# Kernel tuning notes

Hardware: AMD Instinct MI355X
Metric: run time of the kernel (lower is better)

## Reference

```python
import jax, jax.numpy as jnp
import numpy as np

C = 256
CQ = C // 4


def setup_inputs() -> dict:
    key = jax.random.key(0)
    ks = jax.random.split(key, 7)
    B, H, W = 4, 64, 64
    x = jax.random.normal(ks[0], (B, C, H, W), dtype=jnp.float32)
    s = 1.0 / np.sqrt(C)
    Wq = jax.random.normal(ks[1], (CQ, C), dtype=jnp.float32) * s
    bq = jnp.zeros((CQ,), dtype=jnp.float32)
    Wk = jax.random.normal(ks[2], (CQ, C), dtype=jnp.float32) * s
    bk = jnp.zeros((CQ,), dtype=jnp.float32)
    Wv = jax.random.normal(ks[3], (C, C), dtype=jnp.float32) * s
    bv = jnp.zeros((C,), dtype=jnp.float32)
    gamma = jnp.zeros((1,), dtype=jnp.float32)
    return {"x": x, "Wq": Wq, "bq": bq, "Wk": Wk, "bk": bk,
            "Wv": Wv, "bv": bv, "gamma": gamma}


def reference(x, Wq, bq, Wk, bk, Wv, bv, gamma):
    B, Cc, Hh, Ww = x.shape
    N = Hh * Ww
    xf = x.reshape(B, Cc, N)                      # [B, C, N]
    # 1x1 convs are channel-mixing matmuls
    q = jnp.einsum('oc,bcn->bon', Wq, xf) + bq[None, :, None]   # [B, C/4, N]
    k = jnp.einsum('oc,bcn->bon', Wk, xf) + bk[None, :, None]   # [B, C/4, N]
    v = jnp.einsum('oc,bcn->bon', Wv, xf) + bv[None, :, None]   # [B, C, N]
    energy = jnp.einsum('bci,bcj->bij', q, k)     # [B, N, N] (unscaled)
    attn = jax.nn.softmax(energy, axis=-1)
    out = jnp.einsum('bcj,bij->bci', v, attn)     # [B, C, N]
    out = out.reshape(B, Cc, Hh, Ww)
    return gamma[0] * out + x
```

## Files before the change

### kernel.cpp

```cpp
#include <hip/hip_runtime.h>
#include <hip/hip_bf16.h>

typedef unsigned short u16;
typedef unsigned int u32;
typedef float f32x4 __attribute__((ext_vector_type(4)));
typedef short s16x8 __attribute__((ext_vector_type(8)));

#define MFMA16(a, b, c) __builtin_amdgcn_mfma_f32_16x16x32_bf16(a, b, c, 0, 0, 0)

#define NN 4096
#define CC 256
#define CQ 64

__device__ __forceinline__ u16 f2bf(float x) {
    union { float f; u32 u; } v; v.f = x;
    return (u16)((v.u + 0x7FFFu + ((v.u >> 16) & 1u)) >> 16);
}
__device__ __forceinline__ float bf2f(u16 u) {
    union { u32 u; float f; } v; v.u = ((u32)u) << 16;
    return v.f;
}
__device__ __forceinline__ void gll16(const void* g, void* l) {
    __builtin_amdgcn_global_load_lds(
        (const __attribute__((address_space(1))) void*)g,
        (__attribute__((address_space(3))) void*)l, 16, 0, 0);
}

__global__ __launch_bounds__(256) void prep(
    const float* __restrict__ x, const float* __restrict__ Wq,
    const float* __restrict__ Wk, const float* __restrict__ Wv,
    u16* __restrict__ xT, u16* __restrict__ wbf)
{
    const int bid = blockIdx.x, t = threadIdx.x;
    if (bid < 1024) {
        __shared__ float tile[64 * 65];
        const int b = bid >> 8, ctile = (bid >> 6) & 3, ntile = bid & 63;
        const int c0 = ctile * 64, n0 = ntile * 64;
        const int cw = t >> 4, nj = (t & 15) * 4;
        for (int it = 0; it < 4; it++) {
            const int ci = it * 16 + cw;
            const float4 v4 = *(const float4*)(x + ((size_t)(b * CC + c0 + ci)) * NN + n0 + nj);
            tile[(nj + 0) * 65 + ci] = v4.x;
            tile[(nj + 1) * 65 + ci] = v4.y;
            tile[(nj + 2) * 65 + ci] = v4.z;
            tile[(nj + 3) * 65 + ci] = v4.w;
        }
        __syncthreads();
        const int r = t >> 2, c16 = (t & 3) * 16;
        union { u16 h[16]; uint4 q[2]; } pk;
        for (int j = 0; j < 16; j++) pk.h[j] = f2bf(tile[r * 65 + c16 + j]);
        u16* dst = xT + ((size_t)(b * NN + n0 + r)) * CC + c0 + c16;
        *(uint4*)dst = pk.q[0];
        *(uint4*)(dst + 8) = pk.q[1];
    } else {
        const int flat = (bid - 1024) * 1024 + t * 4;
        const int o = flat >> 8, c = flat & 255;
        const float* src = (o < 64)  ? (Wq + (size_t)o * CC + c)
                         : (o < 128) ? (Wk + (size_t)(o - 64) * CC + c)
                                     : (Wv + (size_t)(o - 128) * CC + c);
        const float4 v4 = *(const float4*)src;
        union { u16 h[4]; uint2 d; } pk;
        pk.h[0] = f2bf(v4.x); pk.h[1] = f2bf(v4.y);
        pk.h[2] = f2bf(v4.z); pk.h[3] = f2bf(v4.w);
        *(uint2*)(wbf + (size_t)o * CC + c) = pk.d;
    }
}

__global__ __launch_bounds__(512, 4) void qkv(
    const u16* __restrict__ xT, const u16* __restrict__ wbf,
    const float* __restrict__ bq, const float* __restrict__ bk,
    const float* __restrict__ bv,
    u16* __restrict__ qT, u16* __restrict__ kT, u16* __restrict__ v)
{
    __shared__ __align__(16) u16 sm[384 * 64 + 32 * 64];
    u16* Ws = sm;
    u16* Xs = sm + 384 * 64;

    const int bid = blockIdx.x;
    const int b = bid >> 7, n0 = (bid & 127) * 32;
    const int t = threadIdx.x, lane = t & 63, w = t >> 6;
    const int col = lane & 15, quad = lane >> 4;

    f32x4 acc[3][2];
    for (int i = 0; i < 3; i++) { acc[i][0] = f32x4{0,0,0,0}; acc[i][1] = f32x4{0,0,0,0}; }

    for (int cc = 0; cc < 4; cc++) {
        const int c0 = cc * 64;
        for (int m = 0; m < 6; m++) {
            const int g = m * 512 + t;
            const int row = g >> 3, ch = g & 7;
            gll16(wbf + (size_t)row * CC + c0 + ((ch ^ (row & 7)) * 8), Ws + g * 8);
        }
        if (w < 4) {
            const int g = w * 64 + lane;
            const int n = g >> 3, ch = g & 7;
            gll16(xT + ((size_t)(b * NN + n0 + n)) * CC + c0 + ((ch ^ (n & 7)) * 8),
                  Xs + g * 8);
        }
        __syncthreads();
        for (int kk = 0; kk < 2; kk++) {
            s16x8 bx[2];
            for (int nt2 = 0; nt2 < 2; nt2++) {
                const int n = nt2 * 16 + col;
                bx[nt2] = *(const s16x8*)&Xs[n * 64 + (((kk * 4 + quad) ^ (n & 7)) * 8)];
            }
            for (int ot = 0; ot < 3; ot++) {
                const int row = w * 48 + ot * 16 + col;
                const s16x8 a = *(const s16x8*)&Ws[row * 64 + (((kk * 4 + quad) ^ (row & 7)) * 8)];
                acc[ot][0] = MFMA16(a, bx[0], acc[ot][0]);
                acc[ot][1] = MFMA16(a, bx[1], acc[ot][1]);
            }
        }
        __syncthreads();
    }
    for (int ot = 0; ot < 3; ot++) {
        const int og = w * 48 + ot * 16 + quad * 4;
        for (int nt2 = 0; nt2 < 2; nt2++) {
            const int n = n0 + nt2 * 16 + col;
            if (og < 64) {
                union { u16 h[4]; uint2 d; } pk;
                for (int r = 0; r < 4; r++) pk.h[r] = f2bf(acc[ot][nt2][r] + bq[og + r]);
                *(uint2*)(qT + ((size_t)(b * NN + n)) * CQ + og) = pk.d;
            } else if (og < 128) {
                union { u16 h[4]; uint2 d; } pk;
                for (int r = 0; r < 4; r++) pk.h[r] = f2bf(acc[ot][nt2][r] + bk[og - 64 + r]);
                *(uint2*)(kT + ((size_t)(b * NN + n)) * CQ + (og - 64)) = pk.d;
            } else {
                for (int r = 0; r < 4; r++)
                    v[((size_t)(b * CC + og - 128 + r)) * NN + n] =
                        f2bf(acc[ot][nt2][r] + bv[og - 128 + r]);
            }
        }
    }
}

__global__ __launch_bounds__(512, 4) void flash_attn(
    const u16* __restrict__ qT, const u16* __restrict__ kT,
    const u16* __restrict__ v,
    u16* __restrict__ Op0, float* __restrict__ Op1,
    float* __restrict__ lws)
{
    __shared__ __align__(16) u16 sm[24576];
    __shared__ float ls[2][64];

    const int bid = blockIdx.x;
    const int p = bid & 7;
    const int b = p >> 1, jh = p & 1;
    const int n0 = (bid >> 3) * 64;
    const int jb = jh * 2048;
    const int t = threadIdx.x;
    const int lane = t & 63, wv = t >> 6;
    const int col = lane & 15, quad = lane >> 4;
    const int strip = wv & 3, jhi = wv >> 2;
    const int ih = wv >> 2, cq = wv & 3;

    const int swz8 = (quad ^ ((col >> 1) & 3)) * 8;

    s16x8 aq[2];
    {
        const u16* qp = qT + ((size_t)(b * NN + n0 + strip * 16 + col)) * CQ + quad * 8;
        aq[0] = *(const s16x8*)qp;
        aq[1] = *(const s16x8*)(qp + 32);
    }

    f32x4 o_[2][4];
    for (int i = 0; i < 2; i++) for (int j = 0; j < 4; j++) o_[i][j] = f32x4{0,0,0,0};
    float lac[4] = {0.f, 0.f, 0.f, 0.f};

    const int kg = wv * 64 + lane;
    const int krow = kg >> 3;
    const u16* ksrc = kT + ((size_t)(b * NN + jb + krow)) * CQ + (((kg & 7) ^ (krow & 7)) * 8);
    const int kdo = kg * 8;
    const u16* vsrc[2];
    int vdo[2];
    for (int m = 0; m < 2; m++) {
        const int g = m * 512 + t;
        const int row = g >> 2;
        vdo[m] = g * 8;
        vsrc[m] = v + ((size_t)(b * CC + row)) * NN + jb
                    + (((g & 3) ^ ((row >> 1) & 3)) * 8);
    }

    auto issueK = [&](int jt, int kb) {
        if (wv < 4) gll16(ksrc + (size_t)jt * 32 * CQ, sm + kb * 2048 + kdo);
    };
    auto issueV = [&](int jt, int vb) {
        u16* base = sm + 4096 + vb * 8192;
        for (int m = 0; m < 2; m++)
            gll16(vsrc[m] + jt * 32, base + vdo[m]);
    };
    auto S_phase = [&](int kb, int pb) {
        const u16* Kb = sm + kb * 2048;
        u16* Pb = sm + 20480 + pb * 2048;
        f32x4 s = f32x4{0,0,0,0};
        for (int kk = 0; kk < 2; kk++) {
            const int jrow = jhi * 16 + col;
            const s16x8 bk_ = *(const s16x8*)
                &Kb[jrow * 64 + (((kk * 4 + quad) ^ (jrow & 7)) * 8)];
            s = MFMA16(aq[kk], bk_, s);
        }
        const int jch = jhi * 2 + (col >> 3);
        const int jin = col & 7;
        for (int r = 0; r < 4; r++) {
            const float pv = __expf(fminf(s[r], 60.f));
            lac[r] += pv;
            const int rrow = strip * 16 + quad * 4 + r;
            Pb[rrow * 32 + ((jch ^ ((quad * 2 + (r >> 1)) & 3)) * 8) + jin] = f2bf(pv);
        }
    };
    auto PV_phase = [&](int pb, int vb) {
        const u16* Pb = sm + 20480 + pb * 2048;
        const u16* Vb = sm + 4096 + vb * 8192;
        s16x8 pa[2];
        for (int it2 = 0; it2 < 2; it2++)
            pa[it2] = *(const s16x8*)&Pb[((ih * 2 + it2) * 16 + col) * 32 + swz8];
        for (int ct = 0; ct < 4; ct++) {
            const int c = cq * 64 + ct * 16 + col;
            const s16x8 bv_ = *(const s16x8*)&Vb[c * 32 + swz8];
            o_[0][ct] = MFMA16(pa[0], bv_, o_[0][ct]);
            o_[1][ct] = MFMA16(pa[1], bv_, o_[1][ct]);
        }
    };

    issueK(0, 0);
    issueV(0, 0);
    issueK(1, 1);
    __syncthreads();
    S_phase(0, 0);

    int vcur = 0, pcur = 0;
    for (int m = 0; m < 64; m++) {
        __syncthreads();
        issueV((m + 1 < 64) ? m + 1 : 63, vcur ^ 1);
        issueK((m + 2 < 64) ? m + 2 : 63, m & 1);
        PV_phase(pcur, vcur);
        if (m < 63) S_phase((m + 1) & 1, pcur ^ 1);
        vcur ^= 1; pcur ^= 1;
    }

    for (int r = 0; r < 4; r++) {
        float lv = lac[r];
        lv += __shfl_xor(lv, 1, 64);
        lv += __shfl_xor(lv, 2, 64);
        lv += __shfl_xor(lv, 4, 64);
        lv += __shfl_xor(lv, 8, 64);
        lac[r] = lv;
    }
    if (col == 0)
        for (int r = 0; r < 4; r++)
            ls[jhi][strip * 16 + quad * 4 + r] = lac[r];
    __syncthreads();
    if (t < 64)
        lws[(size_t)jh * 4 * NN + (size_t)b * NN + n0 + t] = ls[0][t] + ls[1][t];

    float* Tf = (float*)sm;
    u16*  Tu = sm;
    for (int rd = 0; rd < 2; rd++) {
        if ((cq >> 1) == rd) {
            const int cl = (cq & 1) * 64;
            for (int it2 = 0; it2 < 2; it2++) {
                const int ib = (ih * 2 + it2) * 16 + quad * 4;
                for (int ct = 0; ct < 4; ct++) {
                    const int c = cl + ct * 16 + col;
                    if (jh == 0) {
                        union { u16 h[4]; uint2 d; } pk;
                        for (int r = 0; r < 4; r++) pk.h[r] = f2bf(o_[it2][ct][r]);
                        *(uint2*)&Tu[c * 136 + ib] = pk.d;
                    } else {
                        *(float2*)&Tf[c * 68 + ib] = float2{o_[it2][ct][0], o_[it2][ct][1]};
                        *(float2*)&Tf[c * 68 + ib + 2] = float2{o_[it2][ct][2], o_[it2][ct][3]};
                    }
                }
            }
        }
        __syncthreads();
        const int cl = t >> 2, i0 = (t & 3) * 16;
        const int c = rd * 128 + cl;
        if (jh == 0) {
            u16* dst = Op0 + ((size_t)(b * CC + c)) * NN + n0 + i0;
            *(uint4*)dst       = *(const uint4*)&Tu[cl * 136 + i0];
            *(uint4*)(dst + 8) = *(const uint4*)&Tu[cl * 136 + i0 + 8];
        } else {
            float* dst = Op1 + ((size_t)(b * CC + c)) * NN + n0 + i0;
            for (int k = 0; k < 4; k++)
                *(float4*)(dst + k * 4) = *(const float4*)&Tf[cl * 68 + i0 + k * 4];
        }
        __syncthreads();
    }
}

__global__ __launch_bounds__(256) void combine(
    const float* __restrict__ x, const u16* __restrict__ Op0,
    const float* __restrict__ lws, const float* __restrict__ gamma,
    float* __restrict__ out)
{
    const size_t idx = ((size_t)blockIdx.x * 256 + threadIdx.x) * 4;
    const int b = (int)(idx >> 20);
    const int n = (int)(idx & (NN - 1));
    const float g = gamma[0];
    const float4 xv = *(const float4*)(x + idx);
    const float4 o1 = *(const float4*)(out + idx);
    union { uint2 d; u16 h[4]; } o0;
    o0.d = *(const uint2*)(Op0 + idx);
    const float4 l0 = *(const float4*)(lws + (size_t)b * NN + n);
    const float4 l1 = *(const float4*)(lws + (size_t)4 * NN + (size_t)b * NN + n);
    float4 r;
    r.x = xv.x + g * (bf2f(o0.h[0]) + o1.x) / (l0.x + l1.x);
    r.y = xv.y + g * (bf2f(o0.h[1]) + o1.y) / (l0.y + l1.y);
    r.z = xv.z + g * (bf2f(o0.h[2]) + o1.z) / (l0.z + l1.z);
    r.w = xv.w + g * (bf2f(o0.h[3]) + o1.w) / (l0.w + l1.w);
    *(float4*)(out + idx) = r;
}

extern "C" void kernel_launch(void* const* d_in, const int* in_sizes, int n_in,
                              void* d_out, int out_size, void* d_ws, size_t ws_size,
                              hipStream_t stream)
{
    const float* x     = (const float*)d_in[0];
    const float* Wq    = (const float*)d_in[1];
    const float* bq    = (const float*)d_in[2];
    const float* Wk    = (const float*)d_in[3];
    const float* bk    = (const float*)d_in[4];
    const float* Wv    = (const float*)d_in[5];
    const float* bv    = (const float*)d_in[6];
    const float* gamma = (const float*)d_in[7];
    float* out = (float*)d_out;

    u16* xT  = (u16*)d_ws;
    u16* wbf = xT  + (size_t)4 * NN * CC;
    u16* qTw = wbf + (size_t)384 * CC;
    u16* kTw = qTw + (size_t)4 * NN * CQ;
    u16* vw  = kTw + (size_t)4 * NN * CQ;
    u16* Op0 = xT;
    float* lws = (float*)wbf;

    prep<<<1120, 256, 0, stream>>>(x, Wq, Wk, Wv, xT, wbf);
    qkv<<<512, 512, 0, stream>>>(xT, wbf, bq, bk, bv, qTw, kTw, vw);
    flash_attn<<<512, 512, 0, stream>>>(qTw, kTw, vw, Op0, out, lws);
    combine<<<4096, 256, 0, stream>>>(x, Op0, lws, gamma, out);
}
```

Measured before the change: 167.4 us.

## Double query tile per block and split keys four ways when workspace allows

The flash attention block now covers 128 query rows instead of 64, so each loaded K/V tile feeds twice as many MFMAs. To keep the grid size, the key range is split into four quarters when the workspace is large enough, with two extra bf16 partial-output buffers. The combine kernel sums up to four partial outputs and denominators. This costs more registers per thread, more LDS for P, and extra partial-output traffic in the combine step, and it falls back to a two-way key split when the workspace is small.

```diff
diff --git a/kernel.cpp b/kernel.cpp
--- a/kernel.cpp
+++ b/kernel.cpp
@@ -137,17 +137,22 @@
 __global__ __launch_bounds__(512, 4) void flash_attn(
     const u16* __restrict__ qT, const u16* __restrict__ kT,
     const u16* __restrict__ v,
-    u16* __restrict__ Op0, float* __restrict__ Op1,
-    float* __restrict__ lws)
-{
-    __shared__ __align__(16) u16 sm[24576];
-    __shared__ float ls[2][64];
+    u16* __restrict__ OpA, u16* __restrict__ OpB, u16* __restrict__ OpC,
+    float* __restrict__ Op1, float* __restrict__ lws,
+    int jqshift, int jlen)
+{
+    __shared__ __align__(16) u16 sm[28672];
+    __shared__ float ls[2][128];
 
     const int bid = blockIdx.x;
-    const int p = bid & 7;
-    const int b = p >> 1, jh = p & 1;
-    const int n0 = (bid >> 3) * 64;
-    const int jb = jh * 2048;
+    const int jqn = 1 << (jqshift - 2);
+    const int p = bid & ((1 << jqshift) - 1);
+    const int b = p >> (jqshift - 2);
+    const int jq = p & (jqn - 1);
+    const int n0 = (bid >> jqshift) * 128;
+    const int jb = jq * jlen;
+    const int iters = jlen >> 5;
+
     const int t = threadIdx.x;
     const int lane = t & 63, wv = t >> 6;
     const int col = lane & 15, quad = lane >> 4;
@@ -156,16 +161,17 @@
 
     const int swz8 = (quad ^ ((col >> 1) & 3)) * 8;
 
-    s16x8 aq[2];
-    {
-        const u16* qp = qT + ((size_t)(b * NN + n0 + strip * 16 + col)) * CQ + quad * 8;
-        aq[0] = *(const s16x8*)qp;
-        aq[1] = *(const s16x8*)(qp + 32);
-    }
-
-    f32x4 o_[2][4];
-    for (int i = 0; i < 2; i++) for (int j = 0; j < 4; j++) o_[i][j] = f32x4{0,0,0,0};
-    float lac[4] = {0.f, 0.f, 0.f, 0.f};
+    s16x8 aq[2][2];
+    for (int it2 = 0; it2 < 2; it2++) {
+        const u16* qp = qT + ((size_t)(b * NN + n0 + strip * 32 + it2 * 16 + col)) * CQ + quad * 8;
+        aq[it2][0] = *(const s16x8*)qp;
+        aq[it2][1] = *(const s16x8*)(qp + 32);
+    }
+
+    f32x4 o_[4][4];
+    for (int i = 0; i < 4; i++)
+        for (int j = 0; j < 4; j++) o_[i][j] = f32x4{0,0,0,0};
+    float lac[8] = {0.f,0.f,0.f,0.f,0.f,0.f,0.f,0.f};
 
     const int kg = wv * 64 + lane;
     const int krow = kg >> 3;
@@ -191,34 +197,37 @@
     };
     auto S_phase = [&](int kb, int pb) {
         const u16* Kb = sm + kb * 2048;
-        u16* Pb = sm + 20480 + pb * 2048;
-        f32x4 s = f32x4{0,0,0,0};
-        for (int kk = 0; kk < 2; kk++) {
-            const int jrow = jhi * 16 + col;
-            const s16x8 bk_ = *(const s16x8*)
-                &Kb[jrow * 64 + (((kk * 4 + quad) ^ (jrow & 7)) * 8)];
-            s = MFMA16(aq[kk], bk_, s);
-        }
+        u16* Pb = sm + 20480 + pb * 4096;
+        const int jrow = jhi * 16 + col;
+        const s16x8 bk0 = *(const s16x8*)&Kb[jrow * 64 + ((quad ^ (jrow & 7)) * 8)];
+        const s16x8 bk1 = *(const s16x8*)&Kb[jrow * 64 + (((4 + quad) ^ (jrow & 7)) * 8)];
         const int jch = jhi * 2 + (col >> 3);
         const int jin = col & 7;
-        for (int r = 0; r < 4; r++) {
-            const float pv = __expf(fminf(s[r], 60.f));
-            lac[r] += pv;
-            const int rrow = strip * 16 + quad * 4 + r;
-            Pb[rrow * 32 + ((jch ^ ((quad * 2 + (r >> 1)) & 3)) * 8) + jin] = f2bf(pv);
+        for (int it2 = 0; it2 < 2; it2++) {
+            f32x4 s = f32x4{0,0,0,0};
+            s = MFMA16(aq[it2][0], bk0, s);
+            s = MFMA16(aq[it2][1], bk1, s);
+            for (int r = 0; r < 4; r++) {
+                const float pv = __expf(fminf(s[r], 60.f));
+                lac[it2 * 4 + r] += pv;
+                const int rrow = strip * 32 + it2 * 16 + quad * 4 + r;
+                Pb[rrow * 32 + ((jch ^ ((quad * 2 + (r >> 1)) & 3)) * 8) + jin] = f2bf(pv);
+            }
         }
     };
     auto PV_phase = [&](int pb, int vb) {
-        const u16* Pb = sm + 20480 + pb * 2048;
+        const u16* Pb = sm + 20480 + pb * 4096;
         const u16* Vb = sm + 4096 + vb * 8192;
-        s16x8 pa[2];
-        for (int it2 = 0; it2 < 2; it2++)
-            pa[it2] = *(const s16x8*)&Pb[((ih * 2 + it2) * 16 + col) * 32 + swz8];
+        s16x8 pa[4];
+        for (int it = 0; it < 4; it++)
+            pa[it] = *(const s16x8*)&Pb[(ih * 64 + it * 16 + col) * 32 + swz8];
         for (int ct = 0; ct < 4; ct++) {
             const int c = cq * 64 + ct * 16 + col;
             const s16x8 bv_ = *(const s16x8*)&Vb[c * 32 + swz8];
             o_[0][ct] = MFMA16(pa[0], bv_, o_[0][ct]);
             o_[1][ct] = MFMA16(pa[1], bv_, o_[1][ct]);
+            o_[2][ct] = MFMA16(pa[2], bv_, o_[2][ct]);
+            o_[3][ct] = MFMA16(pa[3], bv_, o_[3][ct]);
         }
     };
 
@@ -229,70 +238,72 @@
     S_phase(0, 0);
 
     int vcur = 0, pcur = 0;
-    for (int m = 0; m < 64; m++) {
-        __syncthreads();
-        issueV((m + 1 < 64) ? m + 1 : 63, vcur ^ 1);
-        issueK((m + 2 < 64) ? m + 2 : 63, m & 1);
+    for (int m = 0; m < iters; m++) {
+        __syncthreads();
+        issueV((m + 1 < iters) ? m + 1 : iters - 1, vcur ^ 1);
+        issueK((m + 2 < iters) ? m + 2 : iters - 1, m & 1);
         PV_phase(pcur, vcur);
-        if (m < 63) S_phase((m + 1) & 1, pcur ^ 1);
+        if (m < iters - 1) S_phase((m + 1) & 1, pcur ^ 1);
         vcur ^= 1; pcur ^= 1;
     }
 
-    for (int r = 0; r < 4; r++) {
-        float lv = lac[r];
+    for (int i = 0; i < 8; i++) {
+        float lv = lac[i];
         lv += __shfl_xor(lv, 1, 64);
         lv += __shfl_xor(lv, 2, 64);
         lv += __shfl_xor(lv, 4, 64);
         lv += __shfl_xor(lv, 8, 64);
-        lac[r] = lv;
+        lac[i] = lv;
     }
     if (col == 0)
-        for (int r = 0; r < 4; r++)
-            ls[jhi][strip * 16 + quad * 4 + r] = lac[r];
+        for (int i = 0; i < 8; i++)
+            ls[jhi][strip * 32 + (i >> 2) * 16 + quad * 4 + (i & 3)] = lac[i];
     __syncthreads();
-    if (t < 64)
-        lws[(size_t)jh * 4 * NN + (size_t)b * NN + n0 + t] = ls[0][t] + ls[1][t];
-
+    if (t < 128)
+        lws[((size_t)(jq * 4 + b)) * NN + n0 + t] = ls[0][t] + ls[1][t];
+
+    const bool isf32 = (jq == jqn - 1);
+    u16* Opd = (jq == 0) ? OpA : (jq == 1) ? OpB : OpC;
     float* Tf = (float*)sm;
     u16*  Tu = sm;
-    for (int rd = 0; rd < 2; rd++) {
-        if ((cq >> 1) == rd) {
-            const int cl = (cq & 1) * 64;
-            for (int it2 = 0; it2 < 2; it2++) {
-                const int ib = (ih * 2 + it2) * 16 + quad * 4;
+    for (int rd = 0; rd < 4; rd++) {
+        if (cq == rd) {
+            for (int it = 0; it < 4; it++) {
+                const int ib = ih * 64 + it * 16 + quad * 4;
                 for (int ct = 0; ct < 4; ct++) {
-                    const int c = cl + ct * 16 + col;
-                    if (jh == 0) {
+                    const int cl = ct * 16 + col;
+                    if (!isf32) {
                         union { u16 h[4]; uint2 d; } pk;
-                        for (int r = 0; r < 4; r++) pk.h[r] = f2bf(o_[it2][ct][r]);
-                        *(uint2*)&Tu[c * 136 + ib] = pk.d;
+                        for (int r = 0; r < 4; r++) pk.h[r] = f2bf(o_[it][ct][r]);
+                        *(uint2*)&Tu[cl * 136 + ib] = pk.d;
                     } else {
-                        *(float2*)&Tf[c * 68 + ib] = float2{o_[it2][ct][0], o_[it2][ct][1]};
-                        *(float2*)&Tf[c * 68 + ib + 2] = float2{o_[it2][ct][2], o_[it2][ct][3]};
+                        *(float2*)&Tf[cl * 132 + ib]     = float2{o_[it][ct][0], o_[it][ct][1]};
+                        *(float2*)&Tf[cl * 132 + ib + 2] = float2{o_[it][ct][2], o_[it][ct][3]};
                     }
                 }
             }
         }
         __syncthreads();
-        const int cl = t >> 2, i0 = (t & 3) * 16;
-        const int c = rd * 128 + cl;
-        if (jh == 0) {
-            u16* dst = Op0 + ((size_t)(b * CC + c)) * NN + n0 + i0;
+        const int cl = t >> 3, i0 = (t & 7) * 16;
+        const int c = rd * 64 + cl;
+        if (!isf32) {
+            u16* dst = Opd + ((size_t)(b * CC + c)) * NN + n0 + i0;
             *(uint4*)dst       = *(const uint4*)&Tu[cl * 136 + i0];
             *(uint4*)(dst + 8) = *(const uint4*)&Tu[cl * 136 + i0 + 8];
         } else {
             float* dst = Op1 + ((size_t)(b * CC + c)) * NN + n0 + i0;
             for (int k = 0; k < 4; k++)
-                *(float4*)(dst + k * 4) = *(const float4*)&Tf[cl * 68 + i0 + k * 4];
+                *(float4*)(dst + k * 4) = *(const float4*)&Tf[cl * 132 + i0 + k * 4];
         }
         __syncthreads();
     }
 }
 
 __global__ __launch_bounds__(256) void combine(
-    const float* __restrict__ x, const u16* __restrict__ Op0,
+    const float* __restrict__ x, const u16* __restrict__ OpA,
+    const u16* __restrict__ OpB, const u16* __restrict__ OpC,
     const float* __restrict__ lws, const float* __restrict__ gamma,
-    float* __restrict__ out)
+    float* __restrict__ out, int jqn)
 {
     const size_t idx = ((size_t)blockIdx.x * 256 + threadIdx.x) * 4;
     const int b = (int)(idx >> 20);
@@ -300,15 +311,30 @@
     const float g = gamma[0];
     const float4 xv = *(const float4*)(x + idx);
     const float4 o1 = *(const float4*)(out + idx);
-    union { uint2 d; u16 h[4]; } o0;
-    o0.d = *(const uint2*)(Op0 + idx);
-    const float4 l0 = *(const float4*)(lws + (size_t)b * NN + n);
-    const float4 l1 = *(const float4*)(lws + (size_t)4 * NN + (size_t)b * NN + n);
+
+    float4 l = *(const float4*)(lws + (size_t)b * NN + n);
+    for (int q = 1; q < jqn; q++) {
+        const float4 lq = *(const float4*)(lws + ((size_t)(q * 4 + b)) * NN + n);
+        l.x += lq.x; l.y += lq.y; l.z += lq.z; l.w += lq.w;
+    }
+
+    float os[4] = {o1.x, o1.y, o1.z, o1.w};
+    {
+        union { uint2 d; u16 h[4]; } pk;
+        pk.d = *(const uint2*)(OpA + idx);
+        for (int r = 0; r < 4; r++) os[r] += bf2f(pk.h[r]);
+    }
+    if (jqn == 4) {
+        union { uint2 d; u16 h[4]; } pb_, pc_;
+        pb_.d = *(const uint2*)(OpB + idx);
+        pc_.d = *(const uint2*)(OpC + idx);
+        for (int r = 0; r < 4; r++) os[r] += bf2f(pb_.h[r]) + bf2f(pc_.h[r]);
+    }
     float4 r;
-    r.x = xv.x + g * (bf2f(o0.h[0]) + o1.x) / (l0.x + l1.x);
-    r.y = xv.y + g * (bf2f(o0.h[1]) + o1.y) / (l0.y + l1.y);
-    r.z = xv.z + g * (bf2f(o0.h[2]) + o1.z) / (l0.z + l1.z);
-    r.w = xv.w + g * (bf2f(o0.h[3]) + o1.w) / (l0.w + l1.w);
+    r.x = xv.x + g * os[0] / l.x;
+    r.y = xv.y + g * os[1] / l.y;
+    r.z = xv.z + g * os[2] / l.z;
+    r.w = xv.w + g * os[3] / l.w;
     *(float4*)(out + idx) = r;
 }
 
@@ -331,11 +357,29 @@
     u16* qTw = wbf + (size_t)384 * CC;
     u16* kTw = qTw + (size_t)4 * NN * CQ;
     u16* vw  = kTw + (size_t)4 * NN * CQ;
-    u16* Op0 = xT;
-    float* lws = (float*)wbf;
+    u16* wend = vw + (size_t)4 * NN * CC;
+    u16* OpA = xT;
+
+    const size_t base_b  = (size_t)(wend - (u16*)d_ws) * 2;
+    const size_t extra_b = 2 * (size_t)4 * NN * CC * 2 + (size_t)16 * NN * 4;
+
+    int jqn, jqshift, jlen;
+    u16 *OpB, *OpC;
+    float* lws;
+    if (ws_size >= base_b + extra_b) {
+        jqn = 4; jqshift = 4; jlen = NN / 4;
+        OpB = wend;
+        OpC = OpB + (size_t)4 * NN * CC;
+        lws = (float*)(OpC + (size_t)4 * NN * CC);
+    } else {
+        jqn = 2; jqshift = 3; jlen = NN / 2;
+        OpB = OpA; OpC = OpA;
+        lws = (float*)wbf;
+    }
 
     prep<<<1120, 256, 0, stream>>>(x, Wq, Wk, Wv, xT, wbf);
     qkv<<<512, 512, 0, stream>>>(xT, wbf, bq, bk, bv, qTw, kTw, vw);
-    flash_attn<<<512, 512, 0, stream>>>(qTw, kTw, vw, Op0, out, lws);
-    combine<<<4096, 256, 0, stream>>>(x, Op0, lws, gamma, out);
-}
+    flash_attn<<<128 * jqn, 512, 0, stream>>>(qTw, kTw, vw, OpA, OpB, OpC,
+                                              out, lws, jqshift, jlen);
+    combine<<<4096, 256, 0, stream>>>(x, OpA, OpB, OpC, lws, gamma, out, jqn);
+}
```

Result: slower. 177.7 us (+6.2%).

## Fuse combine into flash_attn via per-tile atomic last-block-finishes pattern

Applied to the files above, without the earlier changes.

Removes the separate combine kernel launch. Each flash_attn block bumps an atomic counter for its (batch, query tile), and the second of the two key-half blocks to finish does the normalization, residual add and final write for that tile. The counters are zeroed by an extra block in prep. This saves a kernel launch and a pass over the output, at the cost of threadfences, an atomic per block and a combine tail on the later-finishing blocks.

```diff
diff --git a/kernel.cpp b/kernel.cpp
--- a/kernel.cpp
+++ b/kernel.cpp
@@ -29,7 +29,7 @@
 __global__ __launch_bounds__(256) void prep(
     const float* __restrict__ x, const float* __restrict__ Wq,
     const float* __restrict__ Wk, const float* __restrict__ Wv,
-    u16* __restrict__ xT, u16* __restrict__ wbf)
+    u16* __restrict__ xT, u16* __restrict__ wbf, int* __restrict__ flags)
 {
     const int bid = blockIdx.x, t = threadIdx.x;
     if (bid < 1024) {
@@ -52,7 +52,7 @@
         u16* dst = xT + ((size_t)(b * NN + n0 + r)) * CC + c0 + c16;
         *(uint4*)dst = pk.q[0];
         *(uint4*)(dst + 8) = pk.q[1];
-    } else {
+    } else if (bid < 1120) {
         const int flat = (bid - 1024) * 1024 + t * 4;
         const int o = flat >> 8, c = flat & 255;
         const float* src = (o < 64)  ? (Wq + (size_t)o * CC + c)
@@ -63,6 +63,8 @@
         pk.h[0] = f2bf(v4.x); pk.h[1] = f2bf(v4.y);
         pk.h[2] = f2bf(v4.z); pk.h[3] = f2bf(v4.w);
         *(uint2*)(wbf + (size_t)o * CC + c) = pk.d;
+    } else {
+        flags[t] = 0;
     }
 }
 
@@ -138,10 +140,13 @@
     const u16* __restrict__ qT, const u16* __restrict__ kT,
     const u16* __restrict__ v,
     u16* __restrict__ Op0, float* __restrict__ Op1,
-    float* __restrict__ lws)
+    float* __restrict__ lws,
+    const float* __restrict__ x, const float* __restrict__ gamma,
+    int* __restrict__ flags)
 {
     __shared__ __align__(16) u16 sm[24576];
     __shared__ float ls[2][64];
+    __shared__ int lastFlag;
 
     const int bid = blockIdx.x;
     const int p = bid & 7;
@@ -287,29 +292,35 @@
         }
         __syncthreads();
     }
-}
-
-__global__ __launch_bounds__(256) void combine(
-    const float* __restrict__ x, const u16* __restrict__ Op0,
-    const float* __restrict__ lws, const float* __restrict__ gamma,
-    float* __restrict__ out)
-{
-    const size_t idx = ((size_t)blockIdx.x * 256 + threadIdx.x) * 4;
-    const int b = (int)(idx >> 20);
-    const int n = (int)(idx & (NN - 1));
-    const float g = gamma[0];
-    const float4 xv = *(const float4*)(x + idx);
-    const float4 o1 = *(const float4*)(out + idx);
-    union { uint2 d; u16 h[4]; } o0;
-    o0.d = *(const uint2*)(Op0 + idx);
-    const float4 l0 = *(const float4*)(lws + (size_t)b * NN + n);
-    const float4 l1 = *(const float4*)(lws + (size_t)4 * NN + (size_t)b * NN + n);
-    float4 r;
-    r.x = xv.x + g * (bf2f(o0.h[0]) + o1.x) / (l0.x + l1.x);
-    r.y = xv.y + g * (bf2f(o0.h[1]) + o1.y) / (l0.y + l1.y);
-    r.z = xv.z + g * (bf2f(o0.h[2]) + o1.z) / (l0.z + l1.z);
-    r.w = xv.w + g * (bf2f(o0.h[3]) + o1.w) / (l0.w + l1.w);
-    *(float4*)(out + idx) = r;
+
+    __threadfence();
+    if (t == 0)
+        lastFlag = atomicAdd(&flags[(b << 6) + (bid >> 3)], 1);
+    __syncthreads();
+    if (lastFlag == 1) {
+        __threadfence();
+        const float g = gamma[0];
+        const int c = t >> 1;
+        const int no = n0 + (t & 1) * 32;
+        const size_t rowo = ((size_t)(b * CC + c)) * NN;
+        const float* l0p = lws + (size_t)b * NN;
+        const float* l1p = lws + (size_t)4 * NN + (size_t)b * NN;
+        for (int k = 0; k < 8; k++) {
+            const int n = no + k * 4;
+            const float4 xv = *(const float4*)(x + rowo + n);
+            const float4 o1 = *(const float4*)(Op1 + rowo + n);
+            union { uint2 d; u16 h[4]; } o0;
+            o0.d = *(const uint2*)(Op0 + rowo + n);
+            const float4 l0 = *(const float4*)(l0p + n);
+            const float4 l1 = *(const float4*)(l1p + n);
+            float4 r;
+            r.x = xv.x + g * (bf2f(o0.h[0]) + o1.x) / (l0.x + l1.x);
+            r.y = xv.y + g * (bf2f(o0.h[1]) + o1.y) / (l0.y + l1.y);
+            r.z = xv.z + g * (bf2f(o0.h[2]) + o1.z) / (l0.z + l1.z);
+            r.w = xv.w + g * (bf2f(o0.h[3]) + o1.w) / (l0.w + l1.w);
+            *(float4*)(Op1 + rowo + n) = r;
+        }
+    }
 }
 
 extern "C" void kernel_launch(void* const* d_in, const int* in_sizes, int n_in,
@@ -331,11 +342,12 @@
     u16* qTw = wbf + (size_t)384 * CC;
     u16* kTw = qTw + (size_t)4 * NN * CQ;
     u16* vw  = kTw + (size_t)4 * NN * CQ;
+    int* flags = (int*)(vw + (size_t)4 * NN * CC);
     u16* Op0 = xT;
     float* lws = (float*)wbf;
 
-    prep<<<1120, 256, 0, stream>>>(x, Wq, Wk, Wv, xT, wbf);
+    prep<<<1121, 256, 0, stream>>>(x, Wq, Wk, Wv, xT, wbf, flags);
     qkv<<<512, 512, 0, stream>>>(xT, wbf, bq, bk, bv, qTw, kTw, vw);
-    flash_attn<<<512, 512, 0, stream>>>(qTw, kTw, vw, Op0, out, lws);
-    combine<<<4096, 256, 0, stream>>>(x, Op0, lws, gamma, out);
-}
+    flash_attn<<<512, 512, 0, stream>>>(qTw, kTw, vw, Op0, out, lws,
+                                        x, gamma, flags);
+}
```

Result: slower. 486.7 us (+190.8%).

## Split query rows instead of key range and fuse softmax-normalize epilogue into attention

Applied to the files above, without the earlier changes.

Each block now owns 32 query rows and iterates over all 4096 keys, instead of 64 query rows over half the keys with a separate combine kernel. The softmax normalization, gamma scaling and residual add move into the attention epilogue, which removes the partial-output and row-sum round trips through global memory and one kernel launch. In exchange, only half the waves do the QK^T/exp phase, each block reloads K and V for twice as many tiles relative to its query rows, and the main loop runs twice as many iterations with a barrier in each.

```diff
diff --git a/kernel.cpp b/kernel.cpp
--- a/kernel.cpp
+++ b/kernel.cpp
@@ -137,39 +137,39 @@
 __global__ __launch_bounds__(512, 4) void flash_attn(
     const u16* __restrict__ qT, const u16* __restrict__ kT,
     const u16* __restrict__ v,
-    u16* __restrict__ Op0, float* __restrict__ Op1,
-    float* __restrict__ lws)
+    const float* __restrict__ x, const float* __restrict__ gamma,
+    float* __restrict__ out)
 {
-    __shared__ __align__(16) u16 sm[24576];
-    __shared__ float ls[2][64];
+    __shared__ __align__(16) u16 sm[22528];
+    __shared__ float ls[2][32];
+    __shared__ float lf[32];
 
     const int bid = blockIdx.x;
     const int p = bid & 7;
-    const int b = p >> 1, jh = p & 1;
-    const int n0 = (bid >> 3) * 64;
-    const int jb = jh * 2048;
+    const int b = p >> 1, npar = p & 1;
+    const int n0 = ((bid >> 3) * 2 + npar) * 32;
     const int t = threadIdx.x;
     const int lane = t & 63, wv = t >> 6;
     const int col = lane & 15, quad = lane >> 4;
-    const int strip = wv & 3, jhi = wv >> 2;
-    const int ih = wv >> 2, cq = wv & 3;
+    const int sstrip = wv & 1, sjhi = (wv >> 1) & 1;
+    const int it = wv >> 2, cq = wv & 3;
 
     const int swz8 = (quad ^ ((col >> 1) & 3)) * 8;
 
     s16x8 aq[2];
     {
-        const u16* qp = qT + ((size_t)(b * NN + n0 + strip * 16 + col)) * CQ + quad * 8;
+        const u16* qp = qT + ((size_t)(b * NN + n0 + sstrip * 16 + col)) * CQ + quad * 8;
         aq[0] = *(const s16x8*)qp;
         aq[1] = *(const s16x8*)(qp + 32);
     }
 
-    f32x4 o_[2][4];
-    for (int i = 0; i < 2; i++) for (int j = 0; j < 4; j++) o_[i][j] = f32x4{0,0,0,0};
+    f32x4 o_[4];
+    for (int j = 0; j < 4; j++) o_[j] = f32x4{0,0,0,0};
     float lac[4] = {0.f, 0.f, 0.f, 0.f};
 
     const int kg = wv * 64 + lane;
     const int krow = kg >> 3;
-    const u16* ksrc = kT + ((size_t)(b * NN + jb + krow)) * CQ + (((kg & 7) ^ (krow & 7)) * 8);
+    const u16* ksrc = kT + ((size_t)(b * NN + krow)) * CQ + (((kg & 7) ^ (krow & 7)) * 8);
     const int kdo = kg * 8;
     const u16* vsrc[2];
     int vdo[2];
@@ -177,7 +177,7 @@
         const int g = m * 512 + t;
         const int row = g >> 2;
         vdo[m] = g * 8;
-        vsrc[m] = v + ((size_t)(b * CC + row)) * NN + jb
+        vsrc[m] = v + ((size_t)(b * CC + row)) * NN
                     + (((g & 3) ^ ((row >> 1) & 3)) * 8);
     }
 
@@ -190,35 +190,34 @@
             gll16(vsrc[m] + jt * 32, base + vdo[m]);
     };
     auto S_phase = [&](int kb, int pb) {
-        const u16* Kb = sm + kb * 2048;
-        u16* Pb = sm + 20480 + pb * 2048;
-        f32x4 s = f32x4{0,0,0,0};
-        for (int kk = 0; kk < 2; kk++) {
-            const int jrow = jhi * 16 + col;
-            const s16x8 bk_ = *(const s16x8*)
-                &Kb[jrow * 64 + (((kk * 4 + quad) ^ (jrow & 7)) * 8)];
-            s = MFMA16(aq[kk], bk_, s);
-        }
-        const int jch = jhi * 2 + (col >> 3);
-        const int jin = col & 7;
-        for (int r = 0; r < 4; r++) {
-            const float pv = __expf(fminf(s[r], 60.f));
-            lac[r] += pv;
-            const int rrow = strip * 16 + quad * 4 + r;
-            Pb[rrow * 32 + ((jch ^ ((quad * 2 + (r >> 1)) & 3)) * 8) + jin] = f2bf(pv);
+        if (wv < 4) {
+            const u16* Kb = sm + kb * 2048;
+            u16* Pb = sm + 20480 + pb * 1024;
+            f32x4 s = f32x4{0,0,0,0};
+            for (int kk = 0; kk < 2; kk++) {
+                const int jrow = sjhi * 16 + col;
+                const s16x8 bk_ = *(const s16x8*)
+                    &Kb[jrow * 64 + (((kk * 4 + quad) ^ (jrow & 7)) * 8)];
+                s = MFMA16(aq[kk], bk_, s);
+            }
+            const int jch = sjhi * 2 + (col >> 3);
+            const int jin = col & 7;
+            for (int r = 0; r < 4; r++) {
+                const float pv = __expf(fminf(s[r], 60.f));
+                lac[r] += pv;
+                const int rrow = sstrip * 16 + quad * 4 + r;
+                Pb[rrow * 32 + ((jch ^ ((quad * 2 + (r >> 1)) & 3)) * 8) + jin] = f2bf(pv);
+            }
         }
     };
     auto PV_phase = [&](int pb, int vb) {
-        const u16* Pb = sm + 20480 + pb * 2048;
+        const u16* Pb = sm + 20480 + pb * 1024;
         const u16* Vb = sm + 4096 + vb * 8192;
-        s16x8 pa[2];
-        for (int it2 = 0; it2 < 2; it2++)
-            pa[it2] = *(const s16x8*)&Pb[((ih * 2 + it2) * 16 + col) * 32 + swz8];
+        const s16x8 pa = *(const s16x8*)&Pb[(it * 16 + col) * 32 + swz8];
         for (int ct = 0; ct < 4; ct++) {
             const int c = cq * 64 + ct * 16 + col;
             const s16x8 bv_ = *(const s16x8*)&Vb[c * 32 + swz8];
-            o_[0][ct] = MFMA16(pa[0], bv_, o_[0][ct]);
-            o_[1][ct] = MFMA16(pa[1], bv_, o_[1][ct]);
+            o_[ct] = MFMA16(pa, bv_, o_[ct]);
         }
     };
 
@@ -229,12 +228,12 @@
     S_phase(0, 0);
 
     int vcur = 0, pcur = 0;
-    for (int m = 0; m < 64; m++) {
-        __syncthreads();
-        issueV((m + 1 < 64) ? m + 1 : 63, vcur ^ 1);
-        issueK((m + 2 < 64) ? m + 2 : 63, m & 1);
+    for (int m = 0; m < 128; m++) {
+        __syncthreads();
+        issueV((m + 1 < 128) ? m + 1 : 127, vcur ^ 1);
+        issueK((m + 2 < 128) ? m + 2 : 127, m & 1);
         PV_phase(pcur, vcur);
-        if (m < 63) S_phase((m + 1) & 1, pcur ^ 1);
+        if (m < 127) S_phase((m + 1) & 1, pcur ^ 1);
         vcur ^= 1; pcur ^= 1;
     }
 
@@ -246,70 +245,39 @@
         lv += __shfl_xor(lv, 8, 64);
         lac[r] = lv;
     }
-    if (col == 0)
+    if (wv < 4 && col == 0)
         for (int r = 0; r < 4; r++)
-            ls[jhi][strip * 16 + quad * 4 + r] = lac[r];
+            ls[sjhi][sstrip * 16 + quad * 4 + r] = lac[r];
     __syncthreads();
-    if (t < 64)
-        lws[(size_t)jh * 4 * NN + (size_t)b * NN + n0 + t] = ls[0][t] + ls[1][t];
-
+    if (t < 32) lf[t] = ls[0][t] + ls[1][t];
+    __syncthreads();
+
+    const float g = gamma[0];
     float* Tf = (float*)sm;
-    u16*  Tu = sm;
-    for (int rd = 0; rd < 2; rd++) {
-        if ((cq >> 1) == rd) {
-            const int cl = (cq & 1) * 64;
-            for (int it2 = 0; it2 < 2; it2++) {
-                const int ib = (ih * 2 + it2) * 16 + quad * 4;
-                for (int ct = 0; ct < 4; ct++) {
-                    const int c = cl + ct * 16 + col;
-                    if (jh == 0) {
-                        union { u16 h[4]; uint2 d; } pk;
-                        for (int r = 0; r < 4; r++) pk.h[r] = f2bf(o_[it2][ct][r]);
-                        *(uint2*)&Tu[c * 136 + ib] = pk.d;
-                    } else {
-                        *(float2*)&Tf[c * 68 + ib] = float2{o_[it2][ct][0], o_[it2][ct][1]};
-                        *(float2*)&Tf[c * 68 + ib + 2] = float2{o_[it2][ct][2], o_[it2][ct][3]};
-                    }
-                }
-            }
-        }
-        __syncthreads();
-        const int cl = t >> 2, i0 = (t & 3) * 16;
-        const int c = rd * 128 + cl;
-        if (jh == 0) {
-            u16* dst = Op0 + ((size_t)(b * CC + c)) * NN + n0 + i0;
-            *(uint4*)dst       = *(const uint4*)&Tu[cl * 136 + i0];
-            *(uint4*)(dst + 8) = *(const uint4*)&Tu[cl * 136 + i0 + 8];
-        } else {
-            float* dst = Op1 + ((size_t)(b * CC + c)) * NN + n0 + i0;
-            for (int k = 0; k < 4; k++)
-                *(float4*)(dst + k * 4) = *(const float4*)&Tf[cl * 68 + i0 + k * 4];
-        }
-        __syncthreads();
-    }
-}
-
-__global__ __launch_bounds__(256) void combine(
-    const float* __restrict__ x, const u16* __restrict__ Op0,
-    const float* __restrict__ lws, const float* __restrict__ gamma,
-    float* __restrict__ out)
-{
-    const size_t idx = ((size_t)blockIdx.x * 256 + threadIdx.x) * 4;
-    const int b = (int)(idx >> 20);
-    const int n = (int)(idx & (NN - 1));
-    const float g = gamma[0];
-    const float4 xv = *(const float4*)(x + idx);
-    const float4 o1 = *(const float4*)(out + idx);
-    union { uint2 d; u16 h[4]; } o0;
-    o0.d = *(const uint2*)(Op0 + idx);
-    const float4 l0 = *(const float4*)(lws + (size_t)b * NN + n);
-    const float4 l1 = *(const float4*)(lws + (size_t)4 * NN + (size_t)b * NN + n);
-    float4 r;
-    r.x = xv.x + g * (bf2f(o0.h[0]) + o1.x) / (l0.x + l1.x);
-    r.y = xv.y + g * (bf2f(o0.h[1]) + o1.y) / (l0.y + l1.y);
-    r.z = xv.z + g * (bf2f(o0.h[2]) + o1.z) / (l0.z + l1.z);
-    r.w = xv.w + g * (bf2f(o0.h[3]) + o1.w) / (l0.w + l1.w);
-    *(float4*)(out + idx) = r;
+    for (int rd = 0; rd < 4; rd++) {
+        if (cq == rd) {
+            for (int ct = 0; ct < 4; ct++) {
+                const int cl = ct * 16 + col;
+                const int ib = it * 16 + quad * 4;
+                *(float2*)&Tf[cl * 36 + ib]     = float2{o_[ct][0], o_[ct][1]};
+                *(float2*)&Tf[cl * 36 + ib + 2] = float2{o_[ct][2], o_[ct][3]};
+            }
+        }
+        __syncthreads();
+        const int cl = t >> 3, i0 = (t & 7) * 4;
+        const int c = rd * 64 + cl;
+        const size_t rowo = ((size_t)(b * CC + c)) * NN + n0 + i0;
+        const float2 oa = *(const float2*)&Tf[cl * 36 + i0];
+        const float2 ob = *(const float2*)&Tf[cl * 36 + i0 + 2];
+        const float4 xv = *(const float4*)(x + rowo);
+        float4 r;
+        r.x = xv.x + g * oa.x / lf[i0 + 0];
+        r.y = xv.y + g * oa.y / lf[i0 + 1];
+        r.z = xv.z + g * ob.x / lf[i0 + 2];
+        r.w = xv.w + g * ob.y / lf[i0 + 3];
+        *(float4*)(out + rowo) = r;
+        __syncthreads();
+    }
 }
 
 extern "C" void kernel_launch(void* const* d_in, const int* in_sizes, int n_in,
@@ -331,11 +299,8 @@
     u16* qTw = wbf + (size_t)384 * CC;
     u16* kTw = qTw + (size_t)4 * NN * CQ;
     u16* vw  = kTw + (size_t)4 * NN * CQ;
-    u16* Op0 = xT;
-    float* lws = (float*)wbf;
 
     prep<<<1120, 256, 0, stream>>>(x, Wq, Wk, Wv, xT, wbf);
     qkv<<<512, 512, 0, stream>>>(xT, wbf, bq, bk, bv, qTw, kTw, vw);
-    flash_attn<<<512, 512, 0, stream>>>(qTw, kTw, vw, Op0, out, lws);
-    combine<<<4096, 256, 0, stream>>>(x, Op0, lws, gamma, out);
-}
+    flash_attn<<<512, 512, 0, stream>>>(qTw, kTw, vw, x, gamma, out);
+}
```

After: 202.0 us. 1.21x slower.
